# Performance work log

Measured on AMD Instinct MI355X. Metric: run time of the kernel, lower is better.

Reference implementation:

```python
import jax, jax.numpy as jnp
import numpy as np

N_NODES = 100000


def _gcn_norm(edge_index, num_nodes):
    # PyG gcn_norm with add_self_loops=True, symmetric normalization.
    src = jnp.concatenate([edge_index[0], jnp.arange(num_nodes)])
    dst = jnp.concatenate([edge_index[1], jnp.arange(num_nodes)])
    ones = jnp.ones(src.shape[0], dtype=jnp.float32)
    deg = jax.ops.segment_sum(ones, dst, num_segments=num_nodes)
    dinv = jnp.where(deg > 0, jax.lax.rsqrt(deg), 0.0)
    norm = dinv[src] * dinv[dst]  # [E + N]
    return src, dst, norm


def _gcn_conv(x, W, b, src, dst, norm, num_nodes):
    h = x @ W                                  # dense transform first (PyG order)
    msg = h[src] * norm[:, None]               # gather + scale, [E+N, D]
    agg = jax.ops.segment_sum(msg, dst, num_segments=num_nodes)
    return agg + b


def setup_inputs() -> dict:
    key = jax.random.key(0)
    ks = jax.random.split(key, 6)
    F_in, D, C, E = 256, 64, 47, 1200000
    x = jax.random.normal(ks[0], (N_NODES, F_in), dtype=jnp.float32)
    edge_index = jax.random.randint(ks[1], (2, E), 0, N_NODES)
    W1 = jax.random.normal(ks[2], (F_in, D), dtype=jnp.float32) * (1.0 / np.sqrt(F_in))
    b1 = jnp.zeros((D,), dtype=jnp.float32)
    W2 = jax.random.normal(ks[3], (D, C), dtype=jnp.float32) * (1.0 / np.sqrt(D))
    b2 = jnp.zeros((C,), dtype=jnp.float32)
    return {"x": x, "edge_index": edge_index, "W1": W1, "b1": b1, "W2": W2, "b2": b2}


def reference(x, edge_index, W1, b1, W2, b2):
    src, dst, norm = _gcn_norm(edge_index, N_NODES)
    h = jax.nn.relu(_gcn_conv(x, W1, b1, src, dst, norm, N_NODES))
    # dropout: eval mode (training=False) -> identity
    out = _gcn_conv(h, W2, b2, src, dst, norm, N_NODES)
    return jax.nn.log_softmax(out, axis=1)
```

## Files before the change

kernel.cpp:

```cpp
#include <hip/hip_runtime.h>
#include <math.h>

#define NN 100000
#define FIN 256
#define D1 64
#define C2 47
#define S2 48
#define PREPB 76
#define NBKT 391
#define CAP 4096
#define EPB 4096

typedef unsigned short u16;
typedef unsigned int u32;
typedef __attribute__((ext_vector_type(8))) short short8;
typedef __attribute__((ext_vector_type(4))) float floatx4;

__device__ __forceinline__ u16 f2b(float f) {
    union { float f; unsigned u; } v; v.f = f;
    unsigned r = v.u + 0x7FFF + ((v.u >> 16) & 1);
    return (u16)(r >> 16);
}
__device__ __forceinline__ float b2f_lo(u32 p) { union { unsigned u; float f; } v; v.u = p << 16; return v.f; }
__device__ __forceinline__ float b2f_hi(u32 p) { union { unsigned u; float f; } v; v.u = p & 0xFFFF0000u; return v.f; }

__global__ __launch_bounds__(256) void k_prep_bucket(
    const float* __restrict__ W1, const float* __restrict__ W2,
    u16* __restrict__ W1t, u16* __restrict__ W2t,
    const int* __restrict__ src, const int* __restrict__ dst, int E,
    int* __restrict__ bucketCnt, u32* __restrict__ ebuf)
{
    int b = blockIdx.x;
    if (b < PREPB) {
        int i = b * 256 + threadIdx.x;
        if (i < FIN * D1) {
            int c = i >> 8, k = i & 255;
            W1t[i] = f2b(W1[k * D1 + c]);
        } else if (i < FIN * D1 + D1 * S2) {
            int j = i - FIN * D1;
            int c = j >> 6, k = j & 63;
            W2t[j] = (c < C2) ? f2b(W2[k * C2 + c]) : (u16)0;
        }
        return;
    }
    __shared__ int hist[NBKT];
    __shared__ int base[NBKT];
    const int t = threadIdx.x;
    const int blk = b - PREPB;
    for (int i = t; i < NBKT; i += 256) hist[i] = 0;
    __syncthreads();

    int e0 = blk * EPB + t;
    u32 pk[16]; int bk[16], tk[16];
    #pragma unroll
    for (int j = 0; j < 16; ++j) {
        int e = e0 + j * 256;
        bk[j] = -1;
        if (e < E) {
            int d = dst[e];
            bk[j] = d >> 8;
            pk[j] = (u32)src[e] | ((u32)(d & 255) << 17);
            tk[j] = atomicAdd(&hist[bk[j]], 1);
        }
    }
    __syncthreads();
    for (int i = t; i < NBKT; i += 256)
        base[i] = hist[i] ? atomicAdd(&bucketCnt[i], hist[i]) : 0;
    __syncthreads();
    #pragma unroll
    for (int j = 0; j < 16; ++j)
        if (bk[j] >= 0)
            ebuf[(size_t)bk[j] * CAP + base[bk[j]] + tk[j]] = pk[j];
}

__global__ __launch_bounds__(256) void k_csr_ptr(const int* __restrict__ bucketCnt,
                                                 const u32* __restrict__ ebuf,
                                                 int* __restrict__ rowptr,
                                                 float* __restrict__ dinv, int E) {
    __shared__ int sd[256];
    __shared__ int hist[256];
    const int b = blockIdx.x, t = threadIdx.x;
    int v = ((t < b) ? bucketCnt[t] : 0) + ((t + 256 < b) ? bucketCnt[t + 256] : 0);
    sd[t] = v; __syncthreads();
    for (int off = 128; off; off >>= 1) {
        if (t < off) sd[t] += sd[t + off];
        __syncthreads();
    }
    int ebase = sd[0];
    __syncthreads();

    hist[t] = 0;
    __syncthreads();
    const int cnt = bucketCnt[b];
    const u32* eb = ebuf + (size_t)b * CAP;
    for (int i = t; i < cnt; i += 256)
        atomicAdd(&hist[eb[i] >> 17], 1);
    __syncthreads();

    int h = hist[t];
    sd[t] = h; __syncthreads();
    for (int off = 1; off < 256; off <<= 1) {
        int u = (t >= off) ? sd[t - off] : 0;
        __syncthreads();
        sd[t] += u;
        __syncthreads();
    }
    int node = b * 256 + t;
    if (node <= NN) rowptr[node] = ebase + sd[t] - h;
    if (node < NN) dinv[node] = rsqrtf((float)h + 1.0f);
    if (b == 0 && t == 0) rowptr[NN] = E;
}

__global__ __launch_bounds__(256) void k_fill_gemm1(
    const int* __restrict__ bucketCnt, const u32* __restrict__ ebuf,
    const int* __restrict__ rowptr, int* __restrict__ colidx,
    const float* __restrict__ x, const u16* __restrict__ W1t,
    const float* __restrict__ dinv, u16* __restrict__ hs1)
{
    int b = blockIdx.x;
    const int t = threadIdx.x;
    if (b < NBKT) {
        __shared__ int cur[256];
        int node = b * 256 + t;
        cur[t] = (node < NN) ? rowptr[node] : 0;
        __syncthreads();
        const int cnt = bucketCnt[b];
        const u32* eb = ebuf + (size_t)b * CAP;
        for (int i = t; i < cnt; i += 256) {
            u32 p = eb[i];
            int pos = atomicAdd(&cur[p >> 17], 1);
            colidx[pos] = p & 0x1FFFF;
        }
        return;
    }
    __shared__ short As[2][64 * 40];
    __shared__ short Bs[2][64 * 40];
    const int bm = (b - NBKT) * 64;
    const int w = t >> 6, lane = t & 63;
    const int arow = t >> 2;
    const int ak0 = (t & 3) * 8;

    floatx4 acc[4] = {};
    const int gr = bm + arow;
    const bool rowok = gr < NN;
    const float* xrow = x + (size_t)(rowok ? gr : 0) * FIN + ak0;

    float4 v0 = make_float4(0.f,0.f,0.f,0.f), v1 = v0;
    if (rowok) { v0 = *(const float4*)(xrow); v1 = *(const float4*)(xrow + 4); }
    short8 wv = *(const short8*)(W1t + arow * FIN + ak0);
    {
        short8 av;
        av[0]=(short)f2b(v0.x); av[1]=(short)f2b(v0.y); av[2]=(short)f2b(v0.z); av[3]=(short)f2b(v0.w);
        av[4]=(short)f2b(v1.x); av[5]=(short)f2b(v1.y); av[6]=(short)f2b(v1.z); av[7]=(short)f2b(v1.w);
        *(short8*)(&As[0][arow * 40 + ak0]) = av;
        *(short8*)(&Bs[0][arow * 40 + ak0]) = wv;
    }
    __syncthreads();

    int cb_ = 0;
    for (int kt = 32; kt <= FIN; kt += 32) {
        const bool more = kt < FIN;
        float4 n0, n1; short8 nw;
        if (more) {
            if (rowok) { n0 = *(const float4*)(xrow + kt); n1 = *(const float4*)(xrow + kt + 4); }
            else { n0 = make_float4(0.f,0.f,0.f,0.f); n1 = n0; }
            nw = *(const short8*)(W1t + arow * FIN + kt + ak0);
        }
        short8 af = *(const short8*)(&As[cb_][(w * 16 + (lane & 15)) * 40 + (lane >> 4) * 8]);
        #pragma unroll
        for (int cb = 0; cb < 4; ++cb) {
            short8 bv = *(const short8*)(&Bs[cb_][(cb * 16 + (lane & 15)) * 40 + (lane >> 4) * 8]);
            acc[cb] = __builtin_amdgcn_mfma_f32_16x16x32_bf16(af, bv, acc[cb], 0, 0, 0);
        }
        if (!more) break;
        short8 av;
        av[0]=(short)f2b(n0.x); av[1]=(short)f2b(n0.y); av[2]=(short)f2b(n0.z); av[3]=(short)f2b(n0.w);
        av[4]=(short)f2b(n1.x); av[5]=(short)f2b(n1.y); av[6]=(short)f2b(n1.z); av[7]=(short)f2b(n1.w);
        *(short8*)(&As[cb_ ^ 1][arow * 40 + ak0]) = av;
        *(short8*)(&Bs[cb_ ^ 1][arow * 40 + ak0]) = nw;
        __syncthreads();
        cb_ ^= 1;
    }

    #pragma unroll
    for (int cb = 0; cb < 4; ++cb) {
        #pragma unroll
        for (int r = 0; r < 4; ++r) {
            int grow = bm + w * 16 + (lane >> 4) * 4 + r;
            if (grow < NN) {
                float v = acc[cb][r] * dinv[grow];
                hs1[(size_t)grow * D1 + cb * 16 + (lane & 15)] = f2b(v);
            }
        }
    }
}

__global__ __launch_bounds__(256) void k_gather_gemm2(
    const int* __restrict__ rowptr, const int* __restrict__ colidx,
    const float* __restrict__ dinv, const u16* __restrict__ hs1,
    const float* __restrict__ b1, const u16* __restrict__ W2t,
    u16* __restrict__ hs2)
{
    __shared__ short As[2][64 * 40];
    __shared__ short Bs[2][48 * 40];
    const int t = threadIdx.x;
    const int bm = blockIdx.x * 64;
    const int w = t >> 6;
    const int g8 = (t >> 3) & 7;
    const int l8 = t & 7;

    for (int s = t; s < 384; s += 256) {
        int kt = s / 192, rem = s - kt * 192;
        int r = rem >> 2, j = rem & 3;
        *(short8*)(&Bs[kt][r * 40 + j * 8]) =
            *(const short8*)(W2t + r * D1 + kt * 32 + j * 8);
    }

    {
        const int col = 8 * l8;
        const int kth = l8 >> 2;
        const int cs  = col & 31;
        float4 bbl = *(const float4*)(b1 + col);
        float4 bbh = *(const float4*)(b1 + col + 4);
        #pragma unroll 1
        for (int i = 0; i < 2; ++i) {
            int rl = w * 16 + g8 * 2 + i;
            int node = bm + rl;
            if (node >= NN) break;
            int beg = rowptr[node], end = rowptr[node + 1];
            uint4 sp = *((const uint4*)(hs1 + (size_t)node * D1) + l8);
            float a0=b2f_lo(sp.x), a1=b2f_hi(sp.x), a2=b2f_lo(sp.y), a3=b2f_hi(sp.y);
            float a4=b2f_lo(sp.z), a5=b2f_hi(sp.z), a6=b2f_lo(sp.w), a7=b2f_hi(sp.w);
            float c0=0.f,c1=0.f,c2=0.f,c3=0.f,c4=0.f,c5=0.f,c6=0.f,c7=0.f;
            int e = beg;
            for (; e + 4 <= end; e += 4) {
                int s0 = colidx[e+0], s1 = colidx[e+1], s2 = colidx[e+2], s3 = colidx[e+3];
                uint4 p0 = *((const uint4*)(hs1 + (size_t)s0 * D1) + l8);
                uint4 p1 = *((const uint4*)(hs1 + (size_t)s1 * D1) + l8);
                uint4 p2 = *((const uint4*)(hs1 + (size_t)s2 * D1) + l8);
                uint4 p3 = *((const uint4*)(hs1 + (size_t)s3 * D1) + l8);
                a0+=b2f_lo(p0.x); a1+=b2f_hi(p0.x); a2+=b2f_lo(p0.y); a3+=b2f_hi(p0.y);
                a4+=b2f_lo(p0.z); a5+=b2f_hi(p0.z); a6+=b2f_lo(p0.w); a7+=b2f_hi(p0.w);
                c0+=b2f_lo(p1.x); c1+=b2f_hi(p1.x); c2+=b2f_lo(p1.y); c3+=b2f_hi(p1.y);
                c4+=b2f_lo(p1.z); c5+=b2f_hi(p1.z); c6+=b2f_lo(p1.w); c7+=b2f_hi(p1.w);
                a0+=b2f_lo(p2.x); a1+=b2f_hi(p2.x); a2+=b2f_lo(p2.y); a3+=b2f_hi(p2.y);
                a4+=b2f_lo(p2.z); a5+=b2f_hi(p2.z); a6+=b2f_lo(p2.w); a7+=b2f_hi(p2.w);
                c0+=b2f_lo(p3.x); c1+=b2f_hi(p3.x); c2+=b2f_lo(p3.y); c3+=b2f_hi(p3.y);
                c4+=b2f_lo(p3.z); c5+=b2f_hi(p3.z); c6+=b2f_lo(p3.w); c7+=b2f_hi(p3.w);
            }
            for (; e < end; ++e) {
                uint4 p0 = *((const uint4*)(hs1 + (size_t)colidx[e] * D1) + l8);
                a0+=b2f_lo(p0.x); a1+=b2f_hi(p0.x); a2+=b2f_lo(p0.y); a3+=b2f_hi(p0.y);
                a4+=b2f_lo(p0.z); a5+=b2f_hi(p0.z); a6+=b2f_lo(p0.w); a7+=b2f_hi(p0.w);
            }
            float dd = dinv[node];
            float r0 = fmaxf(fmaf(dd, a0 + c0, bbl.x), 0.f);
            float r1 = fmaxf(fmaf(dd, a1 + c1, bbl.y), 0.f);
            float r2 = fmaxf(fmaf(dd, a2 + c2, bbl.z), 0.f);
            float r3 = fmaxf(fmaf(dd, a3 + c3, bbl.w), 0.f);
            float r4 = fmaxf(fmaf(dd, a4 + c4, bbh.x), 0.f);
            float r5 = fmaxf(fmaf(dd, a5 + c5, bbh.y), 0.f);
            float r6 = fmaxf(fmaf(dd, a6 + c6, bbh.z), 0.f);
            float r7 = fmaxf(fmaf(dd, a7 + c7, bbh.w), 0.f);
            short8 pk;
            pk[0]=(short)f2b(r0); pk[1]=(short)f2b(r1); pk[2]=(short)f2b(r2); pk[3]=(short)f2b(r3);
            pk[4]=(short)f2b(r4); pk[5]=(short)f2b(r5); pk[6]=(short)f2b(r6); pk[7]=(short)f2b(r7);
            *(short8*)(&As[kth][rl * 40 + cs]) = pk;
        }
    }
    __syncthreads();

    const int lane = t & 63;
    floatx4 acc[3] = {};
    #pragma unroll
    for (int kt = 0; kt < 2; ++kt) {
        short8 af = *(const short8*)(&As[kt][(w * 16 + (lane & 15)) * 40 + (lane >> 4) * 8]);
        #pragma unroll
        for (int cb = 0; cb < 3; ++cb) {
            short8 bv = *(const short8*)(&Bs[kt][(cb * 16 + (lane & 15)) * 40 + (lane >> 4) * 8]);
            acc[cb] = __builtin_amdgcn_mfma_f32_16x16x32_bf16(af, bv, acc[cb], 0, 0, 0);
        }
    }

    #pragma unroll
    for (int cb = 0; cb < 3; ++cb) {
        #pragma unroll
        for (int r = 0; r < 4; ++r) {
            int grow = bm + w * 16 + (lane >> 4) * 4 + r;
            if (grow < NN) {
                float v = acc[cb][r] * dinv[grow];
                hs2[(size_t)grow * S2 + cb * 16 + (lane & 15)] = f2b(v);
            }
        }
    }
}

__global__ __launch_bounds__(256) void k_gather47_sm(const int* __restrict__ rowptr,
                                                     const int* __restrict__ colidx,
                                                     const float* __restrict__ dinv,
                                                     const u16* __restrict__ hs,
                                                     const float* __restrict__ b2,
                                                     float* __restrict__ out) {
    int node = blockIdx.x * 32 + (threadIdx.x >> 3);
    int l8 = threadIdx.x & 7;
    if (node >= NN) return;
    bool act = l8 < 6;
    int lc = act ? l8 : 0;
    int beg = rowptr[node], end = rowptr[node + 1];
    uint4 sp = *((const uint4*)(hs + (size_t)node * S2) + lc);
    float a0=b2f_lo(sp.x), a1=b2f_hi(sp.x), a2=b2f_lo(sp.y), a3=b2f_hi(sp.y);
    float a4=b2f_lo(sp.z), a5=b2f_hi(sp.z), a6=b2f_lo(sp.w), a7=b2f_hi(sp.w);
    float c0=0.f,c1=0.f,c2=0.f,c3=0.f,c4=0.f,c5=0.f,c6=0.f,c7=0.f;
    int e = beg;
    for (; e + 4 <= end; e += 4) {
        int s0 = colidx[e+0], s1 = colidx[e+1], s2 = colidx[e+2], s3 = colidx[e+3];
        uint4 p0 = *((const uint4*)(hs + (size_t)s0 * S2) + lc);
        uint4 p1 = *((const uint4*)(hs + (size_t)s1 * S2) + lc);
        uint4 p2 = *((const uint4*)(hs + (size_t)s2 * S2) + lc);
        uint4 p3 = *((const uint4*)(hs + (size_t)s3 * S2) + lc);
        a0+=b2f_lo(p0.x); a1+=b2f_hi(p0.x); a2+=b2f_lo(p0.y); a3+=b2f_hi(p0.y);
        a4+=b2f_lo(p0.z); a5+=b2f_hi(p0.z); a6+=b2f_lo(p0.w); a7+=b2f_hi(p0.w);
        c0+=b2f_lo(p1.x); c1+=b2f_hi(p1.x); c2+=b2f_lo(p1.y); c3+=b2f_hi(p1.y);
        c4+=b2f_lo(p1.z); c5+=b2f_hi(p1.z); c6+=b2f_lo(p1.w); c7+=b2f_hi(p1.w);
        a0+=b2f_lo(p2.x); a1+=b2f_hi(p2.x); a2+=b2f_lo(p2.y); a3+=b2f_hi(p2.y);
        a4+=b2f_lo(p2.z); a5+=b2f_hi(p2.z); a6+=b2f_lo(p2.w); a7+=b2f_hi(p2.w);
        c0+=b2f_lo(p3.x); c1+=b2f_hi(p3.x); c2+=b2f_lo(p3.y); c3+=b2f_hi(p3.y);
        c4+=b2f_lo(p3.z); c5+=b2f_hi(p3.z); c6+=b2f_lo(p3.w); c7+=b2f_hi(p3.w);
    }
    for (; e < end; ++e) {
        uint4 p0 = *((const uint4*)(hs + (size_t)colidx[e] * S2) + lc);
        a0+=b2f_lo(p0.x); a1+=b2f_hi(p0.x); a2+=b2f_lo(p0.y); a3+=b2f_hi(p0.y);
        a4+=b2f_lo(p0.z); a5+=b2f_hi(p0.z); a6+=b2f_lo(p0.w); a7+=b2f_hi(p0.w);
    }
    float dd = dinv[node];
    float fv[8] = { a0+c0, a1+c1, a2+c2, a3+c3, a4+c4, a5+c5, a6+c6, a7+c7 };
    const int fb = 8 * lc;
    float val[8];
    float m = -INFINITY;
    #pragma unroll
    for (int k = 0; k < 8; ++k) {
        int fe = fb + k;
        bool valid = act && (fe < C2);
        val[k] = valid ? fmaf(dd, fv[k], b2[valid ? fe : 0]) : -INFINITY;
        m = fmaxf(m, val[k]);
    }
    #pragma unroll
    for (int off = 1; off < 8; off <<= 1) m = fmaxf(m, __shfl_xor(m, off));
    float ex = 0.f;
    #pragma unroll
    for (int k = 0; k < 8; ++k)
        if (val[k] > -INFINITY) ex += expf(val[k] - m);
    #pragma unroll
    for (int off = 1; off < 8; off <<= 1) ex += __shfl_xor(ex, off);
    float ls = m + logf(ex);
    #pragma unroll
    for (int k = 0; k < 8; ++k) {
        int fe = fb + k;
        if (act && fe < C2) out[(size_t)node * C2 + fe] = val[k] - ls;
    }
}

extern "C" void kernel_launch(void* const* d_in, const int* in_sizes, int n_in,
                              void* d_out, int out_size, void* d_ws, size_t ws_size,
                              hipStream_t stream) {
    const float* x  = (const float*)d_in[0];
    const int*   ei = (const int*)d_in[1];
    const float* W1 = (const float*)d_in[2];
    const float* b1 = (const float*)d_in[3];
    const float* W2 = (const float*)d_in[4];
    const float* b2 = (const float*)d_in[5];
    float* out = (float*)d_out;

    const int E = in_sizes[1] / 2;
    const int* src = ei;
    const int* dst = ei + E;

    char* ws = (char*)d_ws;
    float* dinv      = (float*)(ws);
    int*   bucketCnt = (int*)(ws + 0x80000);
    int*   rowptr    = (int*)(ws + 0x100000);
    u16*   W1t       = (u16*)(ws + 0x180000);
    u16*   W2t       = (u16*)(ws + 0x189000);
    u32*   ebuf      = (u32*)(ws + 0x200000);
    int*   colidx    = (int*)(ws + 0x900000);
    u16*   hs1       = (u16*)(ws + 0xE00000);
    u16*   hs2       = (u16*)(ws + 0x1B00000);

    const int nBk1 = (E + EPB - 1) / EPB;
    const int gb1  = (NN + 63) / 64;

    hipMemsetAsync(bucketCnt, 0, NBKT * sizeof(int), stream);
    k_prep_bucket<<<PREPB + nBk1, 256, 0, stream>>>(W1, W2, W1t, W2t, src, dst, E,
                                                    bucketCnt, ebuf);
    k_csr_ptr<<<NBKT, 256, 0, stream>>>(bucketCnt, ebuf, rowptr, dinv, E);
    k_fill_gemm1<<<NBKT + gb1, 256, 0, stream>>>(bucketCnt, ebuf, rowptr, colidx,
                                                 x, W1t, dinv, hs1);
    k_gather_gemm2<<<gb1, 256, 0, stream>>>(rowptr, colidx, dinv, hs1, b1, W2t, hs2);
    k_gather47_sm<<<(NN + 31) / 32, 256, 0, stream>>>(rowptr, colidx, dinv, hs2, b2, out);
}
```

Baseline: 134.8 us.

## Replace global CSR build with per-block LDS bucket sort of 64-node buckets

Buckets now cover 64 destination nodes instead of 256, with a capacity of 1024 edges each. This removes the separate CSR pointer kernel and the global colidx scatter. Degree and dinv are computed inside the GEMM1 kernel from the bucket histogram. Each gather kernel re-sorts its own bucket in LDS into a local row pointer and column list, and this is done redundantly in both aggregation passes. It cuts one launch and a round-trip of the edge list through global memory. In exchange it adds duplicated sorting work, and any bucket that overflows the fixed capacity has its extra edges silently dropped.

```diff
diff --git a/kernel.cpp b/kernel.cpp
--- a/kernel.cpp
+++ b/kernel.cpp
@@ -7,8 +7,8 @@
 #define C2 47
 #define S2 48
 #define PREPB 76
-#define NBKT 391
-#define CAP 4096
+#define NBKT 1563
+#define CAP 1024
 #define EPB 4096
 
 typedef unsigned short u16;
@@ -58,8 +58,8 @@
         bk[j] = -1;
         if (e < E) {
             int d = dst[e];
-            bk[j] = d >> 8;
-            pk[j] = (u32)src[e] | ((u32)(d & 255) << 17);
+            bk[j] = d >> 6;
+            pk[j] = (u32)src[e] | ((u32)(d & 63) << 17);
             tk[j] = atomicAdd(&hist[bk[j]], 1);
         }
     }
@@ -69,73 +69,40 @@
     __syncthreads();
     #pragma unroll
     for (int j = 0; j < 16; ++j)
-        if (bk[j] >= 0)
-            ebuf[(size_t)bk[j] * CAP + base[bk[j]] + tk[j]] = pk[j];
-}
-
-__global__ __launch_bounds__(256) void k_csr_ptr(const int* __restrict__ bucketCnt,
-                                                 const u32* __restrict__ ebuf,
-                                                 int* __restrict__ rowptr,
-                                                 float* __restrict__ dinv, int E) {
-    __shared__ int sd[256];
-    __shared__ int hist[256];
-    const int b = blockIdx.x, t = threadIdx.x;
-    int v = ((t < b) ? bucketCnt[t] : 0) + ((t + 256 < b) ? bucketCnt[t + 256] : 0);
-    sd[t] = v; __syncthreads();
-    for (int off = 128; off; off >>= 1) {
-        if (t < off) sd[t] += sd[t + off];
-        __syncthreads();
-    }
-    int ebase = sd[0];
-    __syncthreads();
-
-    hist[t] = 0;
-    __syncthreads();
-    const int cnt = bucketCnt[b];
-    const u32* eb = ebuf + (size_t)b * CAP;
-    for (int i = t; i < cnt; i += 256)
-        atomicAdd(&hist[eb[i] >> 17], 1);
-    __syncthreads();
-
-    int h = hist[t];
-    sd[t] = h; __syncthreads();
-    for (int off = 1; off < 256; off <<= 1) {
-        int u = (t >= off) ? sd[t - off] : 0;
-        __syncthreads();
-        sd[t] += u;
-        __syncthreads();
-    }
-    int node = b * 256 + t;
-    if (node <= NN) rowptr[node] = ebase + sd[t] - h;
-    if (node < NN) dinv[node] = rsqrtf((float)h + 1.0f);
-    if (b == 0 && t == 0) rowptr[NN] = E;
-}
-
-__global__ __launch_bounds__(256) void k_fill_gemm1(
+        if (bk[j] >= 0) {
+            int pos = base[bk[j]] + tk[j];
+            if (pos < CAP) ebuf[(size_t)bk[j] * CAP + pos] = pk[j];
+        }
+}
+
+__global__ __launch_bounds__(256) void k_gemm1(
     const int* __restrict__ bucketCnt, const u32* __restrict__ ebuf,
-    const int* __restrict__ rowptr, int* __restrict__ colidx,
     const float* __restrict__ x, const u16* __restrict__ W1t,
-    const float* __restrict__ dinv, u16* __restrict__ hs1)
+    float* __restrict__ dinv, u16* __restrict__ hs1)
 {
-    int b = blockIdx.x;
-    const int t = threadIdx.x;
-    if (b < NBKT) {
-        __shared__ int cur[256];
-        int node = b * 256 + t;
-        cur[t] = (node < NN) ? rowptr[node] : 0;
-        __syncthreads();
-        const int cnt = bucketCnt[b];
-        const u32* eb = ebuf + (size_t)b * CAP;
-        for (int i = t; i < cnt; i += 256) {
-            u32 p = eb[i];
-            int pos = atomicAdd(&cur[p >> 17], 1);
-            colidx[pos] = p & 0x1FFFF;
-        }
-        return;
-    }
     __shared__ short As[2][64 * 40];
     __shared__ short Bs[2][64 * 40];
-    const int bm = (b - NBKT) * 64;
+    __shared__ int hist[64];
+    __shared__ float dinvs[64];
+    const int b = blockIdx.x;
+    const int t = threadIdx.x;
+    const int bm = b * 64;
+
+    if (t < 64) hist[t] = 0;
+    __syncthreads();
+    {
+        int cnt = bucketCnt[b]; if (cnt > CAP) cnt = CAP;
+        const u32* eb = ebuf + (size_t)b * CAP;
+        for (int i = t; i < cnt; i += 256)
+            atomicAdd(&hist[(eb[i] >> 17) & 63], 1);
+    }
+    __syncthreads();
+    if (t < 64) {
+        float dv = rsqrtf((float)hist[t] + 1.0f);
+        dinvs[t] = dv;
+        dinv[bm + t] = dv;
+    }
+
     const int w = t >> 6, lane = t & 63;
     const int arow = t >> 2;
     const int ak0 = (t & 3) * 8;
@@ -186,28 +153,66 @@
     for (int cb = 0; cb < 4; ++cb) {
         #pragma unroll
         for (int r = 0; r < 4; ++r) {
-            int grow = bm + w * 16 + (lane >> 4) * 4 + r;
+            int rl = w * 16 + (lane >> 4) * 4 + r;
+            int grow = bm + rl;
             if (grow < NN) {
-                float v = acc[cb][r] * dinv[grow];
+                float v = acc[cb][r] * dinvs[rl];
                 hs1[(size_t)grow * D1 + cb * 16 + (lane & 15)] = f2b(v);
             }
         }
     }
 }
 
+__device__ __forceinline__ void bucket_sort_lds(
+    const u32* __restrict__ eb, int cnt, int t,
+    u32* elds, u32* sorted, int* hist, int* rp, int* cur)
+{
+    if (t < 64) hist[t] = 0;
+    __syncthreads();
+    for (int i = t; i < cnt; i += 256) {
+        u32 p = eb[i];
+        elds[i] = p;
+        atomicAdd(&hist[(p >> 17) & 63], 1);
+    }
+    __syncthreads();
+    if (t < 64) {
+        int h = hist[t];
+        int v = h;
+        #pragma unroll
+        for (int off = 1; off < 64; off <<= 1) {
+            int u = __shfl_up(v, off);
+            if (t >= off) v += u;
+        }
+        rp[t + 1] = v;
+        cur[t] = v - h;
+        if (t == 0) rp[0] = 0;
+    }
+    __syncthreads();
+    for (int i = t; i < cnt; i += 256) {
+        u32 p = elds[i];
+        int pos = atomicAdd(&cur[(p >> 17) & 63], 1);
+        sorted[pos] = p & 0x1FFFF;
+    }
+    __syncthreads();
+}
+
 __global__ __launch_bounds__(256) void k_gather_gemm2(
-    const int* __restrict__ rowptr, const int* __restrict__ colidx,
+    const int* __restrict__ bucketCnt, const u32* __restrict__ ebuf,
     const float* __restrict__ dinv, const u16* __restrict__ hs1,
     const float* __restrict__ b1, const u16* __restrict__ W2t,
     u16* __restrict__ hs2)
 {
+    __shared__ u32 elds[CAP];
+    __shared__ u32 sorted[CAP];
+    __shared__ int hist[64], rp[65], cur[64];
     __shared__ short As[2][64 * 40];
     __shared__ short Bs[2][48 * 40];
+    __shared__ float dinvs[64];
+    __shared__ float b1s[64];
     const int t = threadIdx.x;
-    const int bm = blockIdx.x * 64;
-    const int w = t >> 6;
-    const int g8 = (t >> 3) & 7;
-    const int l8 = t & 7;
+    const int b = blockIdx.x, bm = b * 64;
+    const int w = t >> 6, lane = t & 63;
+    const int g = t >> 3, l8 = t & 7;
 
     for (int s = t; s < 384; s += 256) {
         int kt = s / 192, rem = s - kt * 192;
@@ -215,26 +220,30 @@
         *(short8*)(&Bs[kt][r * 40 + j * 8]) =
             *(const short8*)(W2t + r * D1 + kt * 32 + j * 8);
     }
+    if (t < 64) { dinvs[t] = dinv[bm + t]; b1s[t] = b1[t]; }
+
+    int cnt = bucketCnt[b]; if (cnt > CAP) cnt = CAP;
+    bucket_sort_lds(ebuf + (size_t)b * CAP, cnt, t, elds, sorted, hist, rp, cur);
 
     {
         const int col = 8 * l8;
         const int kth = l8 >> 2;
         const int cs  = col & 31;
-        float4 bbl = *(const float4*)(b1 + col);
-        float4 bbh = *(const float4*)(b1 + col + 4);
+        float4 bbl = *(const float4*)(b1s + col);
+        float4 bbh = *(const float4*)(b1s + col + 4);
         #pragma unroll 1
         for (int i = 0; i < 2; ++i) {
-            int rl = w * 16 + g8 * 2 + i;
+            int rl = g * 2 + i;
             int node = bm + rl;
             if (node >= NN) break;
-            int beg = rowptr[node], end = rowptr[node + 1];
+            int beg = rp[rl], end = rp[rl + 1];
             uint4 sp = *((const uint4*)(hs1 + (size_t)node * D1) + l8);
             float a0=b2f_lo(sp.x), a1=b2f_hi(sp.x), a2=b2f_lo(sp.y), a3=b2f_hi(sp.y);
             float a4=b2f_lo(sp.z), a5=b2f_hi(sp.z), a6=b2f_lo(sp.w), a7=b2f_hi(sp.w);
             float c0=0.f,c1=0.f,c2=0.f,c3=0.f,c4=0.f,c5=0.f,c6=0.f,c7=0.f;
             int e = beg;
             for (; e + 4 <= end; e += 4) {
-                int s0 = colidx[e+0], s1 = colidx[e+1], s2 = colidx[e+2], s3 = colidx[e+3];
+                int s0 = sorted[e+0], s1 = sorted[e+1], s2 = sorted[e+2], s3 = sorted[e+3];
                 uint4 p0 = *((const uint4*)(hs1 + (size_t)s0 * D1) + l8);
                 uint4 p1 = *((const uint4*)(hs1 + (size_t)s1 * D1) + l8);
                 uint4 p2 = *((const uint4*)(hs1 + (size_t)s2 * D1) + l8);
@@ -249,11 +258,11 @@
                 c4+=b2f_lo(p3.z); c5+=b2f_hi(p3.z); c6+=b2f_lo(p3.w); c7+=b2f_hi(p3.w);
             }
             for (; e < end; ++e) {
-                uint4 p0 = *((const uint4*)(hs1 + (size_t)colidx[e] * D1) + l8);
+                uint4 p0 = *((const uint4*)(hs1 + (size_t)sorted[e] * D1) + l8);
                 a0+=b2f_lo(p0.x); a1+=b2f_hi(p0.x); a2+=b2f_lo(p0.y); a3+=b2f_hi(p0.y);
                 a4+=b2f_lo(p0.z); a5+=b2f_hi(p0.z); a6+=b2f_lo(p0.w); a7+=b2f_hi(p0.w);
             }
-            float dd = dinv[node];
+            float dd = dinvs[rl];
             float r0 = fmaxf(fmaf(dd, a0 + c0, bbl.x), 0.f);
             float r1 = fmaxf(fmaf(dd, a1 + c1, bbl.y), 0.f);
             float r2 = fmaxf(fmaf(dd, a2 + c2, bbl.z), 0.f);
@@ -270,15 +279,14 @@
     }
     __syncthreads();
 
-    const int lane = t & 63;
-    floatx4 acc[3] = {};
+    floatx4 acc2[3] = {};
     #pragma unroll
     for (int kt = 0; kt < 2; ++kt) {
         short8 af = *(const short8*)(&As[kt][(w * 16 + (lane & 15)) * 40 + (lane >> 4) * 8]);
         #pragma unroll
         for (int cb = 0; cb < 3; ++cb) {
             short8 bv = *(const short8*)(&Bs[kt][(cb * 16 + (lane & 15)) * 40 + (lane >> 4) * 8]);
-            acc[cb] = __builtin_amdgcn_mfma_f32_16x16x32_bf16(af, bv, acc[cb], 0, 0, 0);
+            acc2[cb] = __builtin_amdgcn_mfma_f32_16x16x32_bf16(af, bv, acc2[cb], 0, 0, 0);
         }
     }
 
@@ -286,77 +294,95 @@
     for (int cb = 0; cb < 3; ++cb) {
         #pragma unroll
         for (int r = 0; r < 4; ++r) {
-            int grow = bm + w * 16 + (lane >> 4) * 4 + r;
+            int rl2 = w * 16 + (lane >> 4) * 4 + r;
+            int grow = bm + rl2;
             if (grow < NN) {
-                float v = acc[cb][r] * dinv[grow];
+                float v = acc2[cb][r] * dinvs[rl2];
                 hs2[(size_t)grow * S2 + cb * 16 + (lane & 15)] = f2b(v);
             }
         }
     }
 }
 
-__global__ __launch_bounds__(256) void k_gather47_sm(const int* __restrict__ rowptr,
-                                                     const int* __restrict__ colidx,
-                                                     const float* __restrict__ dinv,
-                                                     const u16* __restrict__ hs,
-                                                     const float* __restrict__ b2,
-                                                     float* __restrict__ out) {
-    int node = blockIdx.x * 32 + (threadIdx.x >> 3);
-    int l8 = threadIdx.x & 7;
-    if (node >= NN) return;
-    bool act = l8 < 6;
-    int lc = act ? l8 : 0;
-    int beg = rowptr[node], end = rowptr[node + 1];
-    uint4 sp = *((const uint4*)(hs + (size_t)node * S2) + lc);
-    float a0=b2f_lo(sp.x), a1=b2f_hi(sp.x), a2=b2f_lo(sp.y), a3=b2f_hi(sp.y);
-    float a4=b2f_lo(sp.z), a5=b2f_hi(sp.z), a6=b2f_lo(sp.w), a7=b2f_hi(sp.w);
-    float c0=0.f,c1=0.f,c2=0.f,c3=0.f,c4=0.f,c5=0.f,c6=0.f,c7=0.f;
-    int e = beg;
-    for (; e + 4 <= end; e += 4) {
-        int s0 = colidx[e+0], s1 = colidx[e+1], s2 = colidx[e+2], s3 = colidx[e+3];
-        uint4 p0 = *((const uint4*)(hs + (size_t)s0 * S2) + lc);
-        uint4 p1 = *((const uint4*)(hs + (size_t)s1 * S2) + lc);
-        uint4 p2 = *((const uint4*)(hs + (size_t)s2 * S2) + lc);
-        uint4 p3 = *((const uint4*)(hs + (size_t)s3 * S2) + lc);
-        a0+=b2f_lo(p0.x); a1+=b2f_hi(p0.x); a2+=b2f_lo(p0.y); a3+=b2f_hi(p0.y);
-        a4+=b2f_lo(p0.z); a5+=b2f_hi(p0.z); a6+=b2f_lo(p0.w); a7+=b2f_hi(p0.w);
-        c0+=b2f_lo(p1.x); c1+=b2f_hi(p1.x); c2+=b2f_lo(p1.y); c3+=b2f_hi(p1.y);
-        c4+=b2f_lo(p1.z); c5+=b2f_hi(p1.z); c6+=b2f_lo(p1.w); c7+=b2f_hi(p1.w);
-        a0+=b2f_lo(p2.x); a1+=b2f_hi(p2.x); a2+=b2f_lo(p2.y); a3+=b2f_hi(p2.y);
-        a4+=b2f_lo(p2.z); a5+=b2f_hi(p2.z); a6+=b2f_lo(p2.w); a7+=b2f_hi(p2.w);
-        c0+=b2f_lo(p3.x); c1+=b2f_hi(p3.x); c2+=b2f_lo(p3.y); c3+=b2f_hi(p3.y);
-        c4+=b2f_lo(p3.z); c5+=b2f_hi(p3.z); c6+=b2f_lo(p3.w); c7+=b2f_hi(p3.w);
-    }
-    for (; e < end; ++e) {
-        uint4 p0 = *((const uint4*)(hs + (size_t)colidx[e] * S2) + lc);
-        a0+=b2f_lo(p0.x); a1+=b2f_hi(p0.x); a2+=b2f_lo(p0.y); a3+=b2f_hi(p0.y);
-        a4+=b2f_lo(p0.z); a5+=b2f_hi(p0.z); a6+=b2f_lo(p0.w); a7+=b2f_hi(p0.w);
-    }
-    float dd = dinv[node];
-    float fv[8] = { a0+c0, a1+c1, a2+c2, a3+c3, a4+c4, a5+c5, a6+c6, a7+c7 };
-    const int fb = 8 * lc;
-    float val[8];
-    float m = -INFINITY;
-    #pragma unroll
-    for (int k = 0; k < 8; ++k) {
-        int fe = fb + k;
-        bool valid = act && (fe < C2);
-        val[k] = valid ? fmaf(dd, fv[k], b2[valid ? fe : 0]) : -INFINITY;
-        m = fmaxf(m, val[k]);
-    }
-    #pragma unroll
-    for (int off = 1; off < 8; off <<= 1) m = fmaxf(m, __shfl_xor(m, off));
-    float ex = 0.f;
-    #pragma unroll
-    for (int k = 0; k < 8; ++k)
-        if (val[k] > -INFINITY) ex += expf(val[k] - m);
-    #pragma unroll
-    for (int off = 1; off < 8; off <<= 1) ex += __shfl_xor(ex, off);
-    float ls = m + logf(ex);
-    #pragma unroll
-    for (int k = 0; k < 8; ++k) {
-        int fe = fb + k;
-        if (act && fe < C2) out[(size_t)node * C2 + fe] = val[k] - ls;
+__global__ __launch_bounds__(256) void k_gather47(
+    const int* __restrict__ bucketCnt, const u32* __restrict__ ebuf,
+    const float* __restrict__ dinv, const u16* __restrict__ hs2,
+    const float* __restrict__ b2, float* __restrict__ out)
+{
+    __shared__ u32 elds[CAP];
+    __shared__ u32 sorted[CAP];
+    __shared__ int hist[64], rp[65], cur[64];
+    __shared__ float dinvs[64];
+    __shared__ float b2s[48];
+    const int t = threadIdx.x;
+    const int b = blockIdx.x, bm = b * 64;
+    const int g = t >> 3, l8 = t & 7;
+
+    if (t < 64) dinvs[t] = dinv[bm + t];
+    if (t < 48) b2s[t] = (t < C2) ? b2[t] : 0.f;
+
+    int cnt = bucketCnt[b]; if (cnt > CAP) cnt = CAP;
+    bucket_sort_lds(ebuf + (size_t)b * CAP, cnt, t, elds, sorted, hist, rp, cur);
+
+    const bool act = l8 < 6;
+    const int lc = act ? l8 : 0;
+    #pragma unroll 1
+    for (int i = 0; i < 2; ++i) {
+        int rl = g * 2 + i;
+        int node = bm + rl;
+        if (node >= NN) break;
+        int beg = rp[rl], end = rp[rl + 1];
+        uint4 sp = *((const uint4*)(hs2 + (size_t)node * S2) + lc);
+        float a0=b2f_lo(sp.x), a1=b2f_hi(sp.x), a2=b2f_lo(sp.y), a3=b2f_hi(sp.y);
+        float a4=b2f_lo(sp.z), a5=b2f_hi(sp.z), a6=b2f_lo(sp.w), a7=b2f_hi(sp.w);
+        float c0=0.f,c1=0.f,c2=0.f,c3=0.f,c4=0.f,c5=0.f,c6=0.f,c7=0.f;
+        int e = beg;
+        for (; e + 4 <= end; e += 4) {
+            int s0 = sorted[e+0], s1 = sorted[e+1], s2 = sorted[e+2], s3 = sorted[e+3];
+            uint4 p0 = *((const uint4*)(hs2 + (size_t)s0 * S2) + lc);
+            uint4 p1 = *((const uint4*)(hs2 + (size_t)s1 * S2) + lc);
+            uint4 p2 = *((const uint4*)(hs2 + (size_t)s2 * S2) + lc);
+            uint4 p3 = *((const uint4*)(hs2 + (size_t)s3 * S2) + lc);
+            a0+=b2f_lo(p0.x); a1+=b2f_hi(p0.x); a2+=b2f_lo(p0.y); a3+=b2f_hi(p0.y);
+            a4+=b2f_lo(p0.z); a5+=b2f_hi(p0.z); a6+=b2f_lo(p0.w); a7+=b2f_hi(p0.w);
+            c0+=b2f_lo(p1.x); c1+=b2f_hi(p1.x); c2+=b2f_lo(p1.y); c3+=b2f_hi(p1.y);
+            c4+=b2f_lo(p1.z); c5+=b2f_hi(p1.z); c6+=b2f_lo(p1.w); c7+=b2f_hi(p1.w);
+            a0+=b2f_lo(p2.x); a1+=b2f_hi(p2.x); a2+=b2f_lo(p2.y); a3+=b2f_hi(p2.y);
+            a4+=b2f_lo(p2.z); a5+=b2f_hi(p2.z); a6+=b2f_lo(p2.w); a7+=b2f_hi(p2.w);
+            c0+=b2f_lo(p3.x); c1+=b2f_hi(p3.x); c2+=b2f_lo(p3.y); c3+=b2f_hi(p3.y);
+            c4+=b2f_lo(p3.z); c5+=b2f_hi(p3.z); c6+=b2f_lo(p3.w); c7+=b2f_hi(p3.w);
+        }
+        for (; e < end; ++e) {
+            uint4 p0 = *((const uint4*)(hs2 + (size_t)sorted[e] * S2) + lc);
+            a0+=b2f_lo(p0.x); a1+=b2f_hi(p0.x); a2+=b2f_lo(p0.y); a3+=b2f_hi(p0.y);
+            a4+=b2f_lo(p0.z); a5+=b2f_hi(p0.z); a6+=b2f_lo(p0.w); a7+=b2f_hi(p0.w);
+        }
+        float dd = dinvs[rl];
+        float fv[8] = { a0+c0, a1+c1, a2+c2, a3+c3, a4+c4, a5+c5, a6+c6, a7+c7 };
+        const int fb = 8 * lc;
+        float val[8];
+        float m = -INFINITY;
+        #pragma unroll
+        for (int k = 0; k < 8; ++k) {
+            int fe = fb + k;
+            bool valid = act && (fe < C2);
+            val[k] = valid ? fmaf(dd, fv[k], b2s[valid ? fe : 0]) : -INFINITY;
+            m = fmaxf(m, val[k]);
+        }
+        #pragma unroll
+        for (int off = 1; off < 8; off <<= 1) m = fmaxf(m, __shfl_xor(m, off));
+        float ex = 0.f;
+        #pragma unroll
+        for (int k = 0; k < 8; ++k)
+            if (val[k] > -INFINITY) ex += expf(val[k] - m);
+        #pragma unroll
+        for (int off = 1; off < 8; off <<= 1) ex += __shfl_xor(ex, off);
+        float ls = m + logf(ex);
+        #pragma unroll
+        for (int k = 0; k < 8; ++k) {
+            int fe = fb + k;
+            if (act && fe < C2) out[(size_t)node * C2 + fe] = val[k] - ls;
+        }
     }
 }
 
@@ -378,23 +404,18 @@
     char* ws = (char*)d_ws;
     float* dinv      = (float*)(ws);
     int*   bucketCnt = (int*)(ws + 0x80000);
-    int*   rowptr    = (int*)(ws + 0x100000);
     u16*   W1t       = (u16*)(ws + 0x180000);
     u16*   W2t       = (u16*)(ws + 0x189000);
     u32*   ebuf      = (u32*)(ws + 0x200000);
-    int*   colidx    = (int*)(ws + 0x900000);
     u16*   hs1       = (u16*)(ws + 0xE00000);
     u16*   hs2       = (u16*)(ws + 0x1B00000);
 
     const int nBk1 = (E + EPB - 1) / EPB;
-    const int gb1  = (NN + 63) / 64;
 
     hipMemsetAsync(bucketCnt, 0, NBKT * sizeof(int), stream);
     k_prep_bucket<<<PREPB + nBk1, 256, 0, stream>>>(W1, W2, W1t, W2t, src, dst, E,
                                                     bucketCnt, ebuf);
-    k_csr_ptr<<<NBKT, 256, 0, stream>>>(bucketCnt, ebuf, rowptr, dinv, E);
-    k_fill_gemm1<<<NBKT + gb1, 256, 0, stream>>>(bucketCnt, ebuf, rowptr, colidx,
-                                                 x, W1t, dinv, hs1);
-    k_gather_gemm2<<<gb1, 256, 0, stream>>>(rowptr, colidx, dinv, hs1, b1, W2t, hs2);
-    k_gather47_sm<<<(NN + 31) / 32, 256, 0, stream>>>(rowptr, colidx, dinv, hs2, b2, out);
-}
+    k_gemm1<<<NBKT, 256, 0, stream>>>(bucketCnt, ebuf, x, W1t, dinv, hs1);
+    k_gather_gemm2<<<NBKT, 256, 0, stream>>>(bucketCnt, ebuf, dinv, hs1, b1, W2t, hs2);
+    k_gather47<<<NBKT, 256, 0, stream>>>(bucketCnt, ebuf, dinv, hs2, b2, out);
+}
```

Measured after the change: 124.3 us. 1.08x faster.
